# Optimization experiments

Hardware: AMD Instinct MI355X
Metric: run time of the kernel (lower is better)

## Reference

```python
import jax, jax.numpy as jnp
import numpy as np

N_NODES = 50000
N_IN = 512
HIDDEN = 64
N_CLASSES = 40
N_EDGES = 800000


def setup_inputs() -> dict:
    key = jax.random.key(0)
    ks = jax.random.split(key, 8)
    x = jax.random.normal(ks[0], (N_NODES, N_IN), dtype=jnp.float32)
    edge_index = jax.random.randint(ks[1], (2, N_EDGES), 0, N_NODES, dtype=jnp.int64)
    s1 = 1.0 / np.sqrt(N_IN)
    s2 = 1.0 / np.sqrt(HIDDEN)
    W1 = jax.random.uniform(ks[2], (N_IN, HIDDEN), jnp.float32, -s1, s1)
    b1 = jax.random.uniform(ks[3], (HIDDEN,), jnp.float32, -s1, s1)
    W2 = jax.random.uniform(ks[4], (HIDDEN, HIDDEN), jnp.float32, -s2, s2)
    b2 = jax.random.uniform(ks[5], (HIDDEN,), jnp.float32, -s2, s2)
    Wo = jax.random.uniform(ks[6], (HIDDEN, N_CLASSES), jnp.float32, -s2, s2)
    bo = jax.random.uniform(ks[7], (N_CLASSES,), jnp.float32, -s2, s2)
    return {"x": x, "W1": W1, "b1": b1, "W2": W2, "b2": b2,
            "Wo": Wo, "bo": bo, "edge_index": edge_index}


def _gcn_conv(x, W, b, row, col, n_nodes):
    # h = lin(x)
    h = x @ W + b
    # degree over row (with self loops already appended)
    deg = jnp.zeros((n_nodes,), dtype=h.dtype).at[row].add(1.0)
    dis = deg ** -0.5  # deg >= 1 thanks to self loops
    norm = dis[row] * dis[col]  # [E]
    # message: norm * x_j where x_j = h[row] (source); aggregate to col (target)
    msg = norm[:, None] * h[row]  # [E, d]
    return jax.ops.segment_sum(msg, col, num_segments=n_nodes)


def reference(x, W1, b1, W2, b2, Wo, bo, edge_index):
    n = x.shape[0]
    # add_self_loops
    loop = jnp.arange(n, dtype=edge_index.dtype)
    row = jnp.concatenate([edge_index[0], loop])
    col = jnp.concatenate([edge_index[1], loop])
    h = _gcn_conv(x, W1, b1, row, col, n)
    h = jax.nn.relu(h)
    # dropout is identity in eval mode (training=False)
    h = _gcn_conv(h, W2, b2, row, col, n)
    logits = h @ Wo + bo
    return jax.nn.log_softmax(logits, axis=1)
```

## Files before the change

### kernel.cpp

```cpp
#include <hip/hip_runtime.h>
#include <hip/hip_fp16.h>
#include <cstdint>

#define N_NODES   50000
#define N_IN      512
#define HIDDEN    64
#define N_CLASSES 40
#define N_EDGES   800000

#define G_BLOCKS  200
#define EPB       4000
#define NBINS     196
#define SCAN_N    (NBINS * G_BLOCKS)
#define SCAN_NB   ((SCAN_N + 1023) / 1024)

#define OFF_HA    0u
#define OFF_HB    6400000u
#define OFF_DIS   12800000u
#define OFF_OFFS  13000000u
#define OFF_HISTC 13200016u
#define OFF_HISTR 13356816u
#define OFF_BSUM  13513616u
#define OFF_COLS  13514128u
#define OFF_ROWS  16714128u
#define OFF_EPACK 19914128u
#define OFF_W1T   23114128u
#define OFF_W2T   23179664u

typedef __attribute__((ext_vector_type(8))) short short8_t;
typedef __attribute__((ext_vector_type(4))) float f32x4;

__device__ __forceinline__ ushort f2bf(float f) {
    uint u = __float_as_uint(f);
    uint r = (u + 0x7FFFu + ((u >> 16) & 1u)) >> 16;
    return (ushort)r;
}
__device__ __forceinline__ float bf2f(ushort h) {
    return __uint_as_float((uint)h << 16);
}

__global__ __launch_bounds__(256) void hist_k(const int* __restrict__ erow,
                                              const int* __restrict__ ecol,
                                              int* __restrict__ histC,
                                              int* __restrict__ histR) {
    __shared__ int hc[NBINS], hr[NBINS];
    int t = threadIdx.x, b = blockIdx.x;
    if (t < NBINS) { hc[t] = 0; hr[t] = 0; }
    __syncthreads();
    int s = b * EPB;
    for (int i = s + t; i < s + EPB; i += 256) {
        atomicAdd(&hc[ecol[i] >> 8], 1);
        atomicAdd(&hr[erow[i] >> 8], 1);
    }
    __syncthreads();
    if (t < NBINS) {
        histC[t * G_BLOCKS + b] = hc[t];
        histR[t * G_BLOCKS + b] = hr[t];
    }
}

__global__ __launch_bounds__(256) void scan1(int* __restrict__ histC,
                                             int* __restrict__ histR,
                                             int* __restrict__ bsum, int n) {
    int* a  = blockIdx.y ? histR : histC;
    int* bs = bsum + blockIdx.y * 64;
    int t = threadIdx.x;
    int g = blockIdx.x * 1024 + t * 4;
    int v[4];
#pragma unroll
    for (int i = 0; i < 4; i++) v[i] = (g + i < n) ? a[g + i] : 0;
    int s = v[0] + v[1] + v[2] + v[3];
    int lane = t & 63, wid = t >> 6;
    int x = s;
#pragma unroll
    for (int d = 1; d < 64; d <<= 1) {
        int y = __shfl_up(x, d);
        if (lane >= d) x += y;
    }
    __shared__ int wt[4];
    if (lane == 63) wt[wid] = x;
    __syncthreads();
    int wo = 0;
    for (int w = 0; w < wid; w++) wo += wt[w];
    int run = wo + x - s;
#pragma unroll
    for (int i = 0; i < 4; i++) {
        if (g + i < n) a[g + i] = run;
        run += v[i];
    }
    if (t == 255) bs[blockIdx.x] = wo + x;
}

__global__ void scan2(int* bsum, int nb) {
    int* bs = bsum + blockIdx.x * 64;
    int lane = threadIdx.x;
    int v = (lane < nb) ? bs[lane] : 0;
    int x = v;
#pragma unroll
    for (int d = 1; d < 64; d <<= 1) {
        int y = __shfl_up(x, d);
        if (lane >= d) x += y;
    }
    if (lane < nb) bs[lane] = x - v;
}

__global__ __launch_bounds__(256) void scan3(int* __restrict__ histC,
                                             int* __restrict__ histR,
                                             const int* __restrict__ bsum, int n) {
    int* a = blockIdx.y ? histR : histC;
    const int* bs = bsum + blockIdx.y * 64;
    int i = blockIdx.x * 256 + threadIdx.x;
    if (i < n) a[i] += bs[i >> 10];
}

__global__ __launch_bounds__(256) void scatter_k(const int* __restrict__ erow,
                                                 const int* __restrict__ ecol,
                                                 const int* __restrict__ scC,
                                                 const int* __restrict__ scR,
                                                 uint* __restrict__ colSorted,
                                                 int* __restrict__ rowSorted) {
    __shared__ int curC[NBINS], curR[NBINS];
    int t = threadIdx.x, b = blockIdx.x;
    if (t < NBINS) {
        curC[t] = scC[t * G_BLOCKS + b];
        curR[t] = scR[t * G_BLOCKS + b];
    }
    __syncthreads();
    int s = b * EPB;
    for (int i = s + t; i < s + EPB; i += 256) {
        int r = erow[i], c = ecol[i];
        int p = atomicAdd(&curC[c >> 8], 1);
        colSorted[p] = (uint)r | ((uint)c << 16);
        int q = atomicAdd(&curR[r >> 8], 1);
        rowSorted[q] = r;
    }
}

__global__ __launch_bounds__(256) void fine_row(const int* __restrict__ rowSorted,
                                                const int* __restrict__ scR,
                                                float* __restrict__ disv) {
    __shared__ int cnt[256];
    int bin = blockIdx.x, t = threadIdx.x;
    int base = scR[bin * G_BLOCKS];
    int end  = (bin == NBINS - 1) ? N_EDGES : scR[(bin + 1) * G_BLOCKS];
    cnt[t] = 0;
    __syncthreads();
    for (int i = base + t; i < end; i += 256)
        atomicAdd(&cnt[rowSorted[i] & 255], 1);
    __syncthreads();
    int node = bin * 256 + t;
    if (node < N_NODES) disv[node] = rsqrtf((float)(cnt[t] + 1));
}

__global__ __launch_bounds__(256) void fine_col(const uint* __restrict__ colSorted,
                                                const int* __restrict__ scC,
                                                const float* __restrict__ disv,
                                                int* __restrict__ offs,
                                                uint* __restrict__ epack) {
    __shared__ int cnt[256];
    __shared__ int excl[256];
    __shared__ int wt[4];
    int bin = blockIdx.x, t = threadIdx.x;
    int base = scC[bin * G_BLOCKS];
    int end  = (bin == NBINS - 1) ? N_EDGES : scC[(bin + 1) * G_BLOCKS];
    cnt[t] = 0;
    __syncthreads();
    for (int i = base + t; i < end; i += 256)
        atomicAdd(&cnt[(colSorted[i] >> 16) & 255], 1);
    __syncthreads();
    int lane = t & 63, w = t >> 6;
    int v = cnt[t];
    int x = v;
#pragma unroll
    for (int d = 1; d < 64; d <<= 1) {
        int y = __shfl_up(x, d);
        if (lane >= d) x += y;
    }
    if (lane == 63) wt[w] = x;
    __syncthreads();
    int wo = 0;
    for (int u = 0; u < w; u++) wo += wt[u];
    excl[t] = wo + x - v;
    cnt[t] = 0;
    int node = bin * 256 + t;
    if (node <= N_NODES) offs[node] = base + wo + x - v;
    __syncthreads();
    for (int i = base + t; i < end; i += 256) {
        uint pv = colSorted[i];
        int cl = (pv >> 16) & 255;
        int src = (int)(pv & 0xFFFFu);
        int p = base + excl[cl] + atomicAdd(&cnt[cl], 1);
        ushort nb_ = __half_as_ushort(__float2half_rn(disv[src]));
        epack[p] = ((uint)nb_ << 16) | (uint)src;
    }
}

__global__ __launch_bounds__(256) void transpose_w2(const float* __restrict__ W1,
                                                    const float* __restrict__ W2,
                                                    ushort* __restrict__ w1t,
                                                    ushort* __restrict__ w2t) {
    int i = blockIdx.x * 256 + threadIdx.x;
    if (i < N_IN * 64) {
        int k = i >> 6, n = i & 63;
        w1t[n * N_IN + k] = f2bf(W1[i]);
    } else if (i < N_IN * 64 + HIDDEN * 64) {
        int j = i - N_IN * 64;
        int k = j >> 6, n = j & 63;
        w2t[n * HIDDEN + k] = f2bf(W2[j]);
    }
}

template <bool ABF16>
__global__ __launch_bounds__(256) void gemm_mfma(const void* __restrict__ Av,
                                                 const ushort* __restrict__ WT,
                                                 const float* __restrict__ bias,
                                                 ushort* __restrict__ C,
                                                 int M, int K) {
    __shared__ ushort Asb[64][72];
    __shared__ ushort Bsb[64][72];
    int t = threadIdx.x;
    int w = t >> 6, lane = t & 63;
    int wm = w >> 1, wn = w & 1;
    int lr = lane & 15, lg = lane >> 4;
    int blockRow = blockIdx.x * 64;

    f32x4 acc[2][2];
#pragma unroll
    for (int i = 0; i < 2; i++)
#pragma unroll
        for (int j = 0; j < 2; j++) acc[i][j] = (f32x4){0.f, 0.f, 0.f, 0.f};

    for (int kk = 0; kk < K; kk += 64) {
#pragma unroll
        for (int u = 0; u < 2; u++) {
            int idx = t + u * 256;
            int m = idx >> 3;
            int k8 = (idx & 7) * 8;
            int row = blockRow + m;
            short8_t s;
            if (ABF16) {
                const ushort* A16 = (const ushort*)Av;
                if (row < M) s = *(const short8_t*)(A16 + (size_t)row * K + kk + k8);
                else s = (short8_t){0,0,0,0,0,0,0,0};
            } else {
                const float* A32 = (const float*)Av;
                float4 a0, a1;
                if (row < M) {
                    const float* p = A32 + (size_t)row * K + kk + k8;
                    a0 = *(const float4*)p;
                    a1 = *(const float4*)(p + 4);
                } else {
                    a0 = make_float4(0.f, 0.f, 0.f, 0.f);
                    a1 = a0;
                }
                s[0] = (short)f2bf(a0.x); s[1] = (short)f2bf(a0.y);
                s[2] = (short)f2bf(a0.z); s[3] = (short)f2bf(a0.w);
                s[4] = (short)f2bf(a1.x); s[5] = (short)f2bf(a1.y);
                s[6] = (short)f2bf(a1.z); s[7] = (short)f2bf(a1.w);
            }
            *(short8_t*)&Asb[m][k8] = s;
        }
#pragma unroll
        for (int u = 0; u < 2; u++) {
            int idx = t + u * 256;
            int n = idx >> 3;
            int k8 = (idx & 7) * 8;
            short8_t vv = *(const short8_t*)(WT + (size_t)n * K + kk + k8);
            *(short8_t*)&Bsb[n][k8] = vv;
        }
        __syncthreads();
#pragma unroll
        for (int ks = 0; ks < 2; ks++) {
            int k0 = ks * 32 + lg * 8;
            short8_t af[2], bf_[2];
#pragma unroll
            for (int mi = 0; mi < 2; mi++)
                af[mi] = *(const short8_t*)&Asb[wm * 32 + mi * 16 + lr][k0];
#pragma unroll
            for (int ni = 0; ni < 2; ni++)
                bf_[ni] = *(const short8_t*)&Bsb[wn * 32 + ni * 16 + lr][k0];
#pragma unroll
            for (int mi = 0; mi < 2; mi++)
#pragma unroll
                for (int ni = 0; ni < 2; ni++)
                    acc[mi][ni] = __builtin_amdgcn_mfma_f32_16x16x32_bf16(
                        af[mi], bf_[ni], acc[mi][ni], 0, 0, 0);
        }
        __syncthreads();
    }
#pragma unroll
    for (int mi = 0; mi < 2; mi++) {
#pragma unroll
        for (int ni = 0; ni < 2; ni++) {
            int col = wn * 32 + ni * 16 + lr;
            float bv = bias[col];
#pragma unroll
            for (int r = 0; r < 4; r++) {
                int row = blockRow + wm * 32 + mi * 16 + lg * 4 + r;
                if (row < M) C[(size_t)row * 64 + col] = f2bf(acc[mi][ni][r] + bv);
            }
        }
    }
}

__global__ __launch_bounds__(256) void agg_k(const ushort* __restrict__ H,
                                             const int* __restrict__ offs,
                                             const uint* __restrict__ epack,
                                             const float* __restrict__ disv,
                                             ushort* __restrict__ out,
                                             int do_relu) {
    int wv = (blockIdx.x * 256 + threadIdx.x) >> 6;
    int lane = threadIdx.x & 63;
    if (wv >= N_NODES) return;
    float dn = disv[wv];
    float acc = dn * dn * bf2f(H[(size_t)wv * 64 + lane]);
    int s = offs[wv], e = offs[wv + 1];
    int i = s;
    for (; i + 8 <= e; i += 8) {
        uint ep[8]; ushort hv[8];
#pragma unroll
        for (int u = 0; u < 8; u++) ep[u] = epack[i + u];
#pragma unroll
        for (int u = 0; u < 8; u++)
            hv[u] = H[(size_t)(ep[u] & 0xFFFFu) * 64 + lane];
#pragma unroll
        for (int u = 0; u < 8; u++) {
            float w = dn * __half2float(__ushort_as_half((ushort)(ep[u] >> 16)));
            acc = fmaf(w, bf2f(hv[u]), acc);
        }
    }
    int rem = e - i;
    if (rem > 0) {
        uint ep[8]; ushort hv[8];
#pragma unroll
        for (int u = 0; u < 8; u++) ep[u] = epack[(u < rem) ? (i + u) : i];
#pragma unroll
        for (int u = 0; u < 8; u++)
            hv[u] = H[(size_t)(ep[u] & 0xFFFFu) * 64 + lane];
#pragma unroll
        for (int u = 0; u < 8; u++) {
            float w = (u < rem)
                ? dn * __half2float(__ushort_as_half((ushort)(ep[u] >> 16))) : 0.f;
            acc = fmaf(w, bf2f(hv[u]), acc);
        }
    }
    if (do_relu) acc = fmaxf(acc, 0.f);
    out[(size_t)wv * 64 + lane] = f2bf(acc);
}

__global__ __launch_bounds__(256) void agg_out_k(const ushort* __restrict__ H,
                                                 const int* __restrict__ offs,
                                                 const uint* __restrict__ epack,
                                                 const float* __restrict__ disv,
                                                 const float* __restrict__ Wo,
                                                 const float* __restrict__ bo,
                                                 float* __restrict__ out) {
    __shared__ float Wl[HIDDEN * N_CLASSES];
    __shared__ float bl[N_CLASSES];
    for (int i = threadIdx.x; i < HIDDEN * N_CLASSES; i += 256) Wl[i] = Wo[i];
    if (threadIdx.x < N_CLASSES) bl[threadIdx.x] = bo[threadIdx.x];
    __syncthreads();
    int wv = (blockIdx.x * 256 + threadIdx.x) >> 6;
    int lane = threadIdx.x & 63;
    if (wv >= N_NODES) return;
    float dn = disv[wv];
    float acc = dn * dn * bf2f(H[(size_t)wv * 64 + lane]);
    int s = offs[wv], e = offs[wv + 1];
    int i = s;
    for (; i + 8 <= e; i += 8) {
        uint ep[8]; ushort hv[8];
#pragma unroll
        for (int u = 0; u < 8; u++) ep[u] = epack[i + u];
#pragma unroll
        for (int u = 0; u < 8; u++)
            hv[u] = H[(size_t)(ep[u] & 0xFFFFu) * 64 + lane];
#pragma unroll
        for (int u = 0; u < 8; u++) {
            float w = dn * __half2float(__ushort_as_half((ushort)(ep[u] >> 16)));
            acc = fmaf(w, bf2f(hv[u]), acc);
        }
    }
    int rem = e - i;
    if (rem > 0) {
        uint ep[8]; ushort hv[8];
#pragma unroll
        for (int u = 0; u < 8; u++) ep[u] = epack[(u < rem) ? (i + u) : i];
#pragma unroll
        for (int u = 0; u < 8; u++)
            hv[u] = H[(size_t)(ep[u] & 0xFFFFu) * 64 + lane];
#pragma unroll
        for (int u = 0; u < 8; u++) {
            float w = (u < rem)
                ? dn * __half2float(__ushort_as_half((ushort)(ep[u] >> 16))) : 0.f;
            acc = fmaf(w, bf2f(hv[u]), acc);
        }
    }
    float accL = (lane < N_CLASSES) ? bl[lane] : -1e30f;
#pragma unroll
    for (int k = 0; k < HIDDEN; k++) {
        float xb = __shfl(acc, k);
        if (lane < N_CLASSES) accL = fmaf(xb, Wl[k * N_CLASSES + lane], accL);
    }
    float mx = accL;
#pragma unroll
    for (int d = 32; d; d >>= 1) mx = fmaxf(mx, __shfl_xor(mx, d));
    float ex = (lane < N_CLASSES) ? expf(accL - mx) : 0.f;
    float sm = ex;
#pragma unroll
    for (int d = 32; d; d >>= 1) sm += __shfl_xor(sm, d);
    if (lane < N_CLASSES)
        out[(size_t)wv * N_CLASSES + lane] = accL - mx - logf(sm);
}

extern "C" void kernel_launch(void* const* d_in, const int* in_sizes, int n_in,
                              void* d_out, int out_size, void* d_ws, size_t ws_size,
                              hipStream_t stream) {
    const float* x  = (const float*)d_in[0];
    const float* W1 = (const float*)d_in[1];
    const float* b1 = (const float*)d_in[2];
    const float* W2 = (const float*)d_in[3];
    const float* b2 = (const float*)d_in[4];
    const float* Wo = (const float*)d_in[5];
    const float* bo = (const float*)d_in[6];
    const int* ei   = (const int*)d_in[7];
    const int* erow = ei;
    const int* ecol = ei + N_EDGES;

    char* ws = (char*)d_ws;
    ushort* h_a   = (ushort*)(ws + OFF_HA);
    ushort* h_b   = (ushort*)(ws + OFF_HB);
    float* disv   = (float*)(ws + OFF_DIS);
    int*   offs   = (int*)(ws + OFF_OFFS);
    int*   histC  = (int*)(ws + OFF_HISTC);
    int*   histR  = (int*)(ws + OFF_HISTR);
    int*   bsum   = (int*)(ws + OFF_BSUM);
    uint*  colS   = (uint*)(ws + OFF_COLS);
    int*   rowS   = (int*)(ws + OFF_ROWS);
    uint*  epack  = (uint*)(ws + OFF_EPACK);
    ushort* w1t   = (ushort*)(ws + OFF_W1T);
    ushort* w2t   = (ushort*)(ws + OFF_W2T);
    float* outp   = (float*)d_out;

    hist_k<<<G_BLOCKS, 256, 0, stream>>>(erow, ecol, histC, histR);
    scan1<<<dim3(SCAN_NB, 2), 256, 0, stream>>>(histC, histR, bsum, SCAN_N);
    scan2<<<2, 64, 0, stream>>>(bsum, SCAN_NB);
    scan3<<<dim3((SCAN_N + 255) / 256, 2), 256, 0, stream>>>(histC, histR, bsum, SCAN_N);
    scatter_k<<<G_BLOCKS, 256, 0, stream>>>(erow, ecol, histC, histR, colS, rowS);
    fine_row<<<NBINS, 256, 0, stream>>>(rowS, histR, disv);
    fine_col<<<NBINS, 256, 0, stream>>>(colS, histC, disv, offs, epack);

    transpose_w2<<<(N_IN * 64 + HIDDEN * 64 + 255) / 256, 256, 0, stream>>>(W1, W2, w1t, w2t);

    gemm_mfma<false><<<(N_NODES + 63) / 64, 256, 0, stream>>>(x, w1t, b1, h_a, N_NODES, N_IN);
    agg_k<<<(N_NODES + 3) / 4, 256, 0, stream>>>(h_a, offs, epack, disv, h_b, 1);
    gemm_mfma<true><<<(N_NODES + 63) / 64, 256, 0, stream>>>(h_b, w2t, b2, h_a, N_NODES, HIDDEN);
    agg_out_k<<<(N_NODES + 3) / 4, 256, 0, stream>>>(h_a, offs, epack, disv, Wo, bo, outp);
}
```

Before: 171.6 us.

## Gather neighbor rows with 16-byte loads across 8 edges per wavefront

The aggregation kernels are rewritten so each wavefront splits into 8 groups of 8 lanes. Each group handles a different edge and loads 8 bf16 features with one 16-byte load, and partial sums are combined with xor shuffles. The first 32 edges are prefetched up front to raise memory-level parallelism. This replaces the per-lane 2-byte gathers with wider transactions, at the cost of the shuffle reduction and masked loads on low-degree nodes. The two aggregation kernels are merged into one template with a HEAD flag.

```diff
diff --git a/kernel.cpp b/kernel.cpp
--- a/kernel.cpp
+++ b/kernel.cpp
@@ -303,113 +303,105 @@
     }
 }
 
-__global__ __launch_bounds__(256) void agg_k(const ushort* __restrict__ H,
-                                             const int* __restrict__ offs,
-                                             const uint* __restrict__ epack,
-                                             const float* __restrict__ disv,
-                                             ushort* __restrict__ out,
-                                             int do_relu) {
+template <int HEAD>
+__global__ __launch_bounds__(256) void agg_wide(const ushort* __restrict__ H,
+                                                const int* __restrict__ offs,
+                                                const uint* __restrict__ epack,
+                                                const float* __restrict__ disv,
+                                                ushort* __restrict__ outH,
+                                                const float* __restrict__ Wo,
+                                                const float* __restrict__ bo,
+                                                float* __restrict__ outL) {
+    __shared__ float Wl[HEAD ? HIDDEN * N_CLASSES : 1];
+    __shared__ float bl[HEAD ? N_CLASSES : 1];
+    if (HEAD) {
+        for (int i = threadIdx.x; i < HIDDEN * N_CLASSES; i += 256) Wl[i] = Wo[i];
+        if (threadIdx.x < N_CLASSES) bl[threadIdx.x] = bo[threadIdx.x];
+        __syncthreads();
+    }
     int wv = (blockIdx.x * 256 + threadIdx.x) >> 6;
     int lane = threadIdx.x & 63;
     if (wv >= N_NODES) return;
+    int c = lane & 7, g = lane >> 3;
+    int s = offs[wv], e = offs[wv + 1];
     float dn = disv[wv];
-    float acc = dn * dn * bf2f(H[(size_t)wv * 64 + lane]);
-    int s = offs[wv], e = offs[wv + 1];
-    int i = s;
-    for (; i + 8 <= e; i += 8) {
-        uint ep[8]; ushort hv[8];
-#pragma unroll
-        for (int u = 0; u < 8; u++) ep[u] = epack[i + u];
-#pragma unroll
-        for (int u = 0; u < 8; u++)
-            hv[u] = H[(size_t)(ep[u] & 0xFFFFu) * 64 + lane];
-#pragma unroll
-        for (int u = 0; u < 8; u++) {
-            float w = dn * __half2float(__ushort_as_half((ushort)(ep[u] >> 16)));
-            acc = fmaf(w, bf2f(hv[u]), acc);
-        }
-    }
-    int rem = e - i;
-    if (rem > 0) {
-        uint ep[8]; ushort hv[8];
-#pragma unroll
-        for (int u = 0; u < 8; u++) ep[u] = epack[(u < rem) ? (i + u) : i];
-#pragma unroll
-        for (int u = 0; u < 8; u++)
-            hv[u] = H[(size_t)(ep[u] & 0xFFFFu) * 64 + lane];
-#pragma unroll
-        for (int u = 0; u < 8; u++) {
-            float w = (u < rem)
-                ? dn * __half2float(__ushort_as_half((ushort)(ep[u] >> 16))) : 0.f;
-            acc = fmaf(w, bf2f(hv[u]), acc);
-        }
-    }
-    if (do_relu) acc = fmaxf(acc, 0.f);
-    out[(size_t)wv * 64 + lane] = f2bf(acc);
-}
-
-__global__ __launch_bounds__(256) void agg_out_k(const ushort* __restrict__ H,
-                                                 const int* __restrict__ offs,
-                                                 const uint* __restrict__ epack,
-                                                 const float* __restrict__ disv,
-                                                 const float* __restrict__ Wo,
-                                                 const float* __restrict__ bo,
-                                                 float* __restrict__ out) {
-    __shared__ float Wl[HIDDEN * N_CLASSES];
-    __shared__ float bl[N_CLASSES];
-    for (int i = threadIdx.x; i < HIDDEN * N_CLASSES; i += 256) Wl[i] = Wo[i];
-    if (threadIdx.x < N_CLASSES) bl[threadIdx.x] = bo[threadIdx.x];
-    __syncthreads();
-    int wv = (blockIdx.x * 256 + threadIdx.x) >> 6;
-    int lane = threadIdx.x & 63;
-    if (wv >= N_NODES) return;
-    float dn = disv[wv];
-    float acc = dn * dn * bf2f(H[(size_t)wv * 64 + lane]);
-    int s = offs[wv], e = offs[wv + 1];
-    int i = s;
-    for (; i + 8 <= e; i += 8) {
-        uint ep[8]; ushort hv[8];
-#pragma unroll
-        for (int u = 0; u < 8; u++) ep[u] = epack[i + u];
-#pragma unroll
-        for (int u = 0; u < 8; u++)
-            hv[u] = H[(size_t)(ep[u] & 0xFFFFu) * 64 + lane];
-#pragma unroll
-        for (int u = 0; u < 8; u++) {
-            float w = dn * __half2float(__ushort_as_half((ushort)(ep[u] >> 16)));
-            acc = fmaf(w, bf2f(hv[u]), acc);
-        }
-    }
-    int rem = e - i;
-    if (rem > 0) {
-        uint ep[8]; ushort hv[8];
-#pragma unroll
-        for (int u = 0; u < 8; u++) ep[u] = epack[(u < rem) ? (i + u) : i];
-#pragma unroll
-        for (int u = 0; u < 8; u++)
-            hv[u] = H[(size_t)(ep[u] & 0xFFFFu) * 64 + lane];
-#pragma unroll
-        for (int u = 0; u < 8; u++) {
-            float w = (u < rem)
-                ? dn * __half2float(__ushort_as_half((ushort)(ep[u] >> 16))) : 0.f;
-            acc = fmaf(w, bf2f(hv[u]), acc);
-        }
-    }
-    float accL = (lane < N_CLASSES) ? bl[lane] : -1e30f;
-#pragma unroll
-    for (int k = 0; k < HIDDEN; k++) {
-        float xb = __shfl(acc, k);
-        if (lane < N_CLASSES) accL = fmaf(xb, Wl[k * N_CLASSES + lane], accL);
-    }
-    float mx = accL;
-#pragma unroll
-    for (int d = 32; d; d >>= 1) mx = fmaxf(mx, __shfl_xor(mx, d));
-    float ex = (lane < N_CLASSES) ? expf(accL - mx) : 0.f;
-    float sm = ex;
-#pragma unroll
-    for (int d = 32; d; d >>= 1) sm += __shfl_xor(sm, d);
-    if (lane < N_CLASSES)
-        out[(size_t)wv * N_CLASSES + lane] = accL - mx - logf(sm);
+    int cap = (e > s) ? (e - 1) : 0;
+
+    uint4 sf = *(const uint4*)(H + (size_t)wv * 64 + c * 8);
+    int i0 = s + g, i1 = s + 8 + g, i2 = s + 16 + g, i3 = s + 24 + g;
+    uint ep0 = epack[min(i0, cap)];
+    uint ep1 = epack[min(i1, cap)];
+    uint ep2 = epack[min(i2, cap)];
+    uint ep3 = epack[min(i3, cap)];
+
+    uint4 h0 = *(const uint4*)(H + (size_t)(ep0 & 0xFFFFu) * 64 + c * 8);
+    uint4 h1 = *(const uint4*)(H + (size_t)(ep1 & 0xFFFFu) * 64 + c * 8);
+    uint4 h2 = *(const uint4*)(H + (size_t)(ep2 & 0xFFFFu) * 64 + c * 8);
+    uint4 h3 = *(const uint4*)(H + (size_t)(ep3 & 0xFFFFu) * 64 + c * 8);
+
+    float acc[8];
+#pragma unroll
+    for (int j = 0; j < 8; j++) acc[j] = 0.f;
+
+#define ACCUM(hh, ww) do { \
+    float _w = (ww); \
+    acc[0] = fmaf(_w, __uint_as_float((hh).x << 16), acc[0]); \
+    acc[1] = fmaf(_w, __uint_as_float((hh).x & 0xFFFF0000u), acc[1]); \
+    acc[2] = fmaf(_w, __uint_as_float((hh).y << 16), acc[2]); \
+    acc[3] = fmaf(_w, __uint_as_float((hh).y & 0xFFFF0000u), acc[3]); \
+    acc[4] = fmaf(_w, __uint_as_float((hh).z << 16), acc[4]); \
+    acc[5] = fmaf(_w, __uint_as_float((hh).z & 0xFFFF0000u), acc[5]); \
+    acc[6] = fmaf(_w, __uint_as_float((hh).w << 16), acc[6]); \
+    acc[7] = fmaf(_w, __uint_as_float((hh).w & 0xFFFF0000u), acc[7]); \
+} while (0)
+
+#define EPW(ep, ii) (((ii) < e) ? dn * __half2float(__ushort_as_half((ushort)((ep) >> 16))) : 0.f)
+
+    ACCUM(h0, EPW(ep0, i0));
+    ACCUM(h1, EPW(ep1, i1));
+    ACCUM(h2, EPW(ep2, i2));
+    ACCUM(h3, EPW(ep3, i3));
+
+    for (int i = s + 32; i < e; i += 8) {
+        int idx = i + g;
+        uint ep = epack[min(idx, cap)];
+        uint4 hh = *(const uint4*)(H + (size_t)(ep & 0xFFFFu) * 64 + c * 8);
+        ACCUM(hh, EPW(ep, idx));
+    }
+
+#pragma unroll
+    for (int m = 8; m < 64; m <<= 1)
+#pragma unroll
+        for (int j = 0; j < 8; j++) acc[j] += __shfl_xor(acc[j], m);
+
+    ACCUM(sf, dn * dn);
+
+    if (!HEAD) {
+        if (g == 0) {
+            short8_t sv;
+#pragma unroll
+            for (int j = 0; j < 8; j++) sv[j] = (short)f2bf(fmaxf(acc[j], 0.f));
+            *(short8_t*)(outH + (size_t)wv * 64 + c * 8) = sv;
+        }
+    } else {
+        float accL = (lane < N_CLASSES) ? bl[lane] : -1e30f;
+#pragma unroll
+        for (int k = 0; k < HIDDEN; k++) {
+            float xb = __shfl(acc[k & 7], k >> 3);
+            if (lane < N_CLASSES) accL = fmaf(xb, Wl[k * N_CLASSES + lane], accL);
+        }
+        float mx = accL;
+#pragma unroll
+        for (int d = 32; d; d >>= 1) mx = fmaxf(mx, __shfl_xor(mx, d));
+        float ex = (lane < N_CLASSES) ? expf(accL - mx) : 0.f;
+        float sm = ex;
+#pragma unroll
+        for (int d = 32; d; d >>= 1) sm += __shfl_xor(sm, d);
+        if (lane < N_CLASSES)
+            outL[(size_t)wv * N_CLASSES + lane] = accL - mx - logf(sm);
+    }
+#undef ACCUM
+#undef EPW
 }
 
 extern "C" void kernel_launch(void* const* d_in, const int* in_sizes, int n_in,
@@ -452,7 +444,9 @@
     transpose_w2<<<(N_IN * 64 + HIDDEN * 64 + 255) / 256, 256, 0, stream>>>(W1, W2, w1t, w2t);
 
     gemm_mfma<false><<<(N_NODES + 63) / 64, 256, 0, stream>>>(x, w1t, b1, h_a, N_NODES, N_IN);
-    agg_k<<<(N_NODES + 3) / 4, 256, 0, stream>>>(h_a, offs, epack, disv, h_b, 1);
+    agg_wide<0><<<(N_NODES + 3) / 4, 256, 0, stream>>>(h_a, offs, epack, disv, h_b,
+                                                       nullptr, nullptr, nullptr);
     gemm_mfma<true><<<(N_NODES + 63) / 64, 256, 0, stream>>>(h_b, w2t, b2, h_a, N_NODES, HIDDEN);
-    agg_out_k<<<(N_NODES + 3) / 4, 256, 0, stream>>>(h_a, offs, epack, disv, Wo, bo, outp);
-}
+    agg_wide<1><<<(N_NODES + 3) / 4, 256, 0, stream>>>(h_a, offs, epack, disv, nullptr,
+                                                       Wo, bo, outp);
+}
```

Result: no change. 174.8 us (+1.9%).
